# Performance work log

Measured on AMD Instinct MI355X. Metric: run time of the kernel, lower is better.

Reference implementation:

```python
import jax, jax.numpy as jnp
import numpy as np

B, N, D_IN = 128, 128, 1024
H1, D_OUT = 256, 32
K = 8  # num_clusters


def setup_inputs() -> dict:
    key = jax.random.key(0)
    ks = jax.random.split(key, 3)
    x = jax.random.normal(ks[0], (B, N, D_IN), dtype=jnp.float32)
    W1 = jax.random.normal(ks[1], (D_IN, H1), dtype=jnp.float32) * (1.0 / np.sqrt(D_IN))
    b1 = jnp.zeros((H1,), jnp.float32)
    W2 = jax.random.normal(ks[2], (H1, D_OUT), dtype=jnp.float32) * (1.0 / np.sqrt(H1))
    b2 = jnp.zeros((D_OUT,), jnp.float32)
    return {"x": x, "W1": W1, "b1": b1, "W2": W2, "b2": b2}


def _mlp(x, W1, b1, W2, b2):
    # nn.Sequential(GELU, Linear(1024,256), GELU, Linear(256,32)); torch GELU default = exact erf
    h = jax.nn.gelu(x, approximate=False)
    h = h @ W1 + b1
    h = jax.nn.gelu(h, approximate=False)
    return h @ W2 + b2  # [B, N, 32]


def _ward_labels(feats, k):
    """Greedy ward-linkage agglomerative clustering of feats [n, d] -> int labels [n].
    Ward merge cost d(A,B) = |A||B|/(|A|+|B|) * ||c_A - c_B||^2 (Lance-Williams equiv)."""
    n = feats.shape[0]
    eye = jnp.eye(n, dtype=bool)

    def body(t, state):
        cents, sizes, lab = state
        sq = jnp.sum(cents * cents, axis=-1)
        d2 = jnp.maximum(sq[:, None] + sq[None, :] - 2.0 * (cents @ cents.T), 0.0)
        w = (sizes[:, None] * sizes[None, :]) / (sizes[:, None] + sizes[None, :] + 1e-30)
        active = sizes > 0
        valid = (active[:, None] & active[None, :]) & (~eye)
        Dm = jnp.where(valid, w * d2, jnp.inf)
        idx = jnp.argmin(Dm)
        i, j = idx // n, idx % n
        i2 = jnp.minimum(i, j)
        j2 = jnp.maximum(i, j)
        si, sj = sizes[i2], sizes[j2]
        newc = (cents[i2] * si + cents[j2] * sj) / (si + sj)
        cents = cents.at[i2].set(newc)
        sizes = sizes.at[i2].set(si + sj).at[j2].set(0.0)
        lab = jnp.where(lab == j2, i2, lab)
        return cents, sizes, lab

    init = (feats, jnp.ones((n,), feats.dtype), jnp.arange(n))
    cents, sizes, lab = jax.lax.fori_loop(0, n - k, body, init)
    # relabel surviving representative indices to 0..k-1 (ordered by index)
    rank = jnp.cumsum((sizes > 0).astype(jnp.int32)) - 1
    return rank[lab]


def reference(x, W1, b1, W2, b2):
    feats = _mlp(x, W1, b1, W2, b2)          # [B, N, 32]
    labels = jax.vmap(lambda f: _ward_labels(f, K))(feats)  # [B, N] int32
    return labels
```

## Files before the change

kernel.cpp:

```cpp
#include <hip/hip_runtime.h>
#include <math.h>

#define BB 128
#define NN 128
#define DIN 1024
#define H1 256
#define DOUT 32
#define KCL 8
#define NPTS 128
#define MROWS (BB*NN)
#define CSTR 130
#define RSTR 132
#define DEADKEY 0xFFFFFFFF00000000ull

__device__ __forceinline__ float gelu_exact(float v) {
    return 0.5f * v * (1.0f + erff(v * 0.70710678118654752f));
}

__device__ __forceinline__ unsigned long long mkkey(float v, int r, int j) {
    return ((unsigned long long)__float_as_uint(v) << 32) | (unsigned)((r << 7) | j);
}

__device__ __forceinline__ float readlanef(float v, int lane) {
    return __int_as_float(__builtin_amdgcn_readlane(__float_as_int(v), lane));
}

template<int CTRL, int RMASK>
__device__ __forceinline__ unsigned dpp_umin_step(unsigned v) {
    unsigned t = (unsigned)__builtin_amdgcn_update_dpp((int)v, (int)v, CTRL, RMASK, 0xf, false);
    return t < v ? t : v;
}
__device__ __forceinline__ unsigned wave_umin_bcast(unsigned v) {
    v = dpp_umin_step<0x111, 0xf>(v);
    v = dpp_umin_step<0x112, 0xf>(v);
    v = dpp_umin_step<0x114, 0xf>(v);
    v = dpp_umin_step<0x118, 0xf>(v);
    v = dpp_umin_step<0x142, 0xa>(v);
    v = dpp_umin_step<0x143, 0xc>(v);
    return (unsigned)__builtin_amdgcn_readlane((int)v, 63);
}
__device__ __forceinline__ unsigned half_umin(unsigned v) {
    v = dpp_umin_step<0x111, 0xf>(v);
    v = dpp_umin_step<0x112, 0xf>(v);
    v = dpp_umin_step<0x114, 0xf>(v);
    v = dpp_umin_step<0x118, 0xf>(v);
    v = dpp_umin_step<0x142, 0xa>(v);
    return v;
}

__global__ __launch_bounds__(256) void gelu_kernel(const float* __restrict__ x,
                                                   float* __restrict__ gx, int n4) {
    int i = blockIdx.x * 256 + threadIdx.x;
    const int stride = gridDim.x * 256;
    for (; i < n4; i += stride) {
        float4 v = ((const float4*)x)[i];
        v.x = gelu_exact(v.x);
        v.y = gelu_exact(v.y);
        v.z = gelu_exact(v.z);
        v.w = gelu_exact(v.w);
        ((float4*)gx)[i] = v;
    }
}

template<bool FUSE>
__global__ __launch_bounds__(256) void mlp1_kernel(const float* __restrict__ xin,
                                                   const float* __restrict__ W1,
                                                   const float* __restrict__ b1,
                                                   float* __restrict__ h) {
    __shared__ float As[32][68];
    __shared__ float Bs[32][68];
    const int bm = blockIdx.x;
    const int bn = blockIdx.y;
    const int tid = threadIdx.x;
    const int tx = tid & 15, ty = tid >> 4;

    float acc[4][4] = {{0.f}};

    const int arow = tid >> 2;
    const int acol4 = (tid & 3) * 4;
    const int brow = tid >> 4;
    const int bcol4 = (tid & 15) * 4;

    const float* xrow = xin + (size_t)(bm * 64 + arow) * DIN;
    const float* wbase = W1 + bn * 64;

    for (int kt = 0; kt < DIN; kt += 32) {
        float4 a0 = *(const float4*)(xrow + kt + acol4);
        float4 a1 = *(const float4*)(xrow + kt + 16 + acol4);
        float4 w0 = *(const float4*)(wbase + (size_t)(kt + brow) * H1 + bcol4);
        float4 w1 = *(const float4*)(wbase + (size_t)(kt + 16 + brow) * H1 + bcol4);
        __syncthreads();
        if (FUSE) {
            As[acol4 + 0][arow] = gelu_exact(a0.x);
            As[acol4 + 1][arow] = gelu_exact(a0.y);
            As[acol4 + 2][arow] = gelu_exact(a0.z);
            As[acol4 + 3][arow] = gelu_exact(a0.w);
            As[16 + acol4 + 0][arow] = gelu_exact(a1.x);
            As[16 + acol4 + 1][arow] = gelu_exact(a1.y);
            As[16 + acol4 + 2][arow] = gelu_exact(a1.z);
            As[16 + acol4 + 3][arow] = gelu_exact(a1.w);
        } else {
            As[acol4 + 0][arow] = a0.x;
            As[acol4 + 1][arow] = a0.y;
            As[acol4 + 2][arow] = a0.z;
            As[acol4 + 3][arow] = a0.w;
            As[16 + acol4 + 0][arow] = a1.x;
            As[16 + acol4 + 1][arow] = a1.y;
            As[16 + acol4 + 2][arow] = a1.z;
            As[16 + acol4 + 3][arow] = a1.w;
        }
        *(float4*)&Bs[brow][bcol4] = w0;
        *(float4*)&Bs[16 + brow][bcol4] = w1;
        __syncthreads();
#pragma unroll
        for (int kk = 0; kk < 32; ++kk) {
            float4 a = *(const float4*)&As[kk][ty * 4];
            float4 b = *(const float4*)&Bs[kk][tx * 4];
            float ar[4] = {a.x, a.y, a.z, a.w};
            float br[4] = {b.x, b.y, b.z, b.w};
#pragma unroll
            for (int i = 0; i < 4; ++i)
#pragma unroll
                for (int j = 0; j < 4; ++j)
                    acc[i][j] = fmaf(ar[i], br[j], acc[i][j]);
        }
    }

    const int row = bm * 64 + ty * 4;
    const int col = bn * 64 + tx * 4;
    float4 bias = *(const float4*)(b1 + col);
#pragma unroll
    for (int i = 0; i < 4; ++i) {
        float4 o;
        o.x = acc[i][0] + bias.x;
        o.y = acc[i][1] + bias.y;
        o.z = acc[i][2] + bias.z;
        o.w = acc[i][3] + bias.w;
        *(float4*)(h + (size_t)(row + i) * H1 + col) = o;
    }
}

__global__ __launch_bounds__(256) void mlp2_kernel(const float* __restrict__ h,
                                                   const float* __restrict__ W2,
                                                   const float* __restrict__ b2,
                                                   float* __restrict__ feats) {
    __shared__ float hs[16][257];
    __shared__ float w2s[H1 * DOUT];
    const int blk = blockIdx.x;
    const int tid = threadIdx.x;

    for (int i = tid; i < (H1 * DOUT) / 4; i += 256) {
        ((float4*)w2s)[i] = ((const float4*)W2)[i];
    }
    const float* hb = h + (size_t)blk * 16 * H1;
    for (int i = tid; i < (16 * H1) / 4; i += 256) {
        float4 v = ((const float4*)hb)[i];
        int r = i >> 6;
        int c = (i & 63) * 4;
        hs[r][c + 0] = gelu_exact(v.x);
        hs[r][c + 1] = gelu_exact(v.y);
        hs[r][c + 2] = gelu_exact(v.z);
        hs[r][c + 3] = gelu_exact(v.w);
    }
    __syncthreads();

    const int col = tid & 31;
    const int r0 = (tid >> 5) * 2;
    float acc0 = 0.f, acc1 = 0.f;
    for (int k = 0; k < H1; ++k) {
        float w = w2s[k * DOUT + col];
        acc0 = fmaf(hs[r0 + 0][k], w, acc0);
        acc1 = fmaf(hs[r0 + 1][k], w, acc1);
    }
    float bias = b2[col];
    const int rowg = blk * 16 + r0;
    feats[(size_t)(rowg + 0) * DOUT + col] = acc0 + bias;
    feats[(size_t)(rowg + 1) * DOUT + col] = acc1 + bias;
}

__global__ __launch_bounds__(256) void ward_kernel(const float* __restrict__ feats,
                                                   int* __restrict__ out) {
    __shared__ __align__(16) float cost[NPTS * RSTR];
    __shared__ __align__(16) float G[NPTS * RSTR];
    __shared__ float centsT[32 * CSTR];
    __shared__ unsigned long long rowkey[NPTS];
    __shared__ float sqArr[NPTS];
    __shared__ float szsE[NPTS];
    __shared__ int rnk[NPTS];

    const int b = blockIdx.x;
    const int tid = threadIdx.x;
    const float* f = feats + (size_t)b * NPTS * DOUT;
    const float INF = __builtin_inff();

    for (int i = tid; i < NPTS * DOUT; i += 256) {
        int r = i >> 5, d = i & 31;
        centsT[d * CSTR + r] = f[i];
    }
    __syncthreads();
    if (tid < NPTS) {
        float s = 0.f;
#pragma unroll
        for (int d = 0; d < 32; ++d) {
            float v = centsT[d * CSTR + tid];
            s = fmaf(v, v, s);
        }
        sqArr[tid] = s;
    }
    __syncthreads();
    {
        int ti = tid >> 4, tj = tid & 15;
        int I0 = ti * 8, J0 = tj * 8;
        float acc[8][8];
#pragma unroll
        for (int u = 0; u < 8; ++u)
#pragma unroll
            for (int v = 0; v < 8; ++v) acc[u][v] = 0.f;
        for (int d = 0; d < 32; ++d) {
            float a[8], bb[8];
#pragma unroll
            for (int u = 0; u < 8; ++u) a[u] = centsT[d * CSTR + I0 + u];
#pragma unroll
            for (int v = 0; v < 8; ++v) bb[v] = centsT[d * CSTR + J0 + v];
#pragma unroll
            for (int u = 0; u < 8; ++u)
#pragma unroll
                for (int v = 0; v < 8; ++v)
                    acc[u][v] = fmaf(a[u], bb[v], acc[u][v]);
        }
#pragma unroll
        for (int u = 0; u < 8; ++u) {
#pragma unroll
            for (int v = 0; v < 8; ++v) {
                int i = I0 + u, j = J0 + v;
                G[i * RSTR + j] = acc[u][v];
                float d2 = sqArr[i] + sqArr[j] - 2.0f * acc[u][v];
                if (d2 < 0.f) d2 = 0.f;
                float w = (1.0f * 1.0f) / (1.0f + 1.0f + 1e-30f);
                cost[i * RSTR + j] = (i == j) ? INF : w * d2;
            }
        }
    }
    __syncthreads();
    if (tid < NPTS) {
        unsigned long long best = DEADKEY;
        for (int j = 0; j < NPTS; ++j) {
            float v = cost[tid * RSTR + j];
            unsigned long long k = mkkey(v, tid, j);
            if (k < best) best = k;
        }
        rowkey[tid] = best;
    }
    __syncthreads();

    if (tid >= 64) return;
    const int lane = tid;
    const int hh = lane & 31;
    const int r0 = lane * 2, r1 = lane * 2 + 1;

    unsigned long long k0 = rowkey[r0], k1 = rowkey[r1];
    float q0 = sqArr[r0], q1 = sqArr[r1];
    float s0 = 1.0f, s1 = 1.0f;
    int lab0 = r0, lab1 = r1;
    unsigned long long alive0 = ~0ull, alive1 = ~0ull;

    for (int it = 0; it < NPTS - KCL; ++it) {
        unsigned bv0 = (unsigned)(k0 >> 32), bv1 = (unsigned)(k1 >> 32);
        unsigned lmin = bv0 < bv1 ? bv0 : bv1;
        unsigned lflat = (bv0 <= bv1) ? (unsigned)(k0 & 0x3FFFu) : (unsigned)(k1 & 0x3FFFu);
        unsigned gmin = wave_umin_bcast(lmin);
        unsigned long long bmask = __ballot(lmin == gmin);
        int lsel = __ffsll(bmask) - 1;
        unsigned flat = (unsigned)__builtin_amdgcn_readlane((int)lflat, lsel);
        int ra = (int)(flat >> 7), ca = (int)(flat & 127u);
        const int i2 = ra < ca ? ra : ca;
        const int j2 = ra < ca ? ca : ra;

        float2 gi = *(const float2*)&G[i2 * RSTR + r0];
        float2 gj = *(const float2*)&G[j2 * RSTR + r0];

        float si = readlanef((i2 & 1) ? s1 : s0, i2 >> 1);
        float sj = readlanef((j2 & 1) ? s1 : s0, j2 >> 1);
        const float snew = si + sj;
        const float invs = 1.0f / snew;
        const float wa = si * invs, wb = sj * invs;

        int arg0 = (int)(k0 & 127u), arg1 = (int)(k1 & 127u);
        bool d0 = (s0 > 0.f) && r0 != i2 && r0 != j2 && (arg0 == i2 || arg0 == j2);
        bool d1 = (s1 > 0.f) && r1 != i2 && r1 != j2 && (arg1 == i2 || arg1 == j2);
        unsigned long long m0 = __ballot(d0), m1 = __ballot(d1);

        float Gii = readlanef((i2 & 1) ? gi.y : gi.x, i2 >> 1);
        float Gij = readlanef((i2 & 1) ? gj.y : gj.x, i2 >> 1);
        float Gjj = readlanef((j2 & 1) ? gj.y : gj.x, j2 >> 1);
        float dotA = wa * Gii + wb * Gij;
        float dotB = wa * Gij + wb * Gjj;
        float qn = wa * dotA + wb * dotB;

        float dot0 = wa * gi.x + wb * gj.x;
        float dot1 = wa * gi.y + wb * gj.y;

        if (lab0 == j2) lab0 = i2;
        if (lab1 == j2) lab1 = i2;
        if (r0 == i2) s0 = snew; else if (r0 == j2) { s0 = 0.f; k0 = DEADKEY; }
        if (r1 == i2) s1 = snew; else if (r1 == j2) { s1 = 0.f; k1 = DEADKEY; }
        if (j2 < 64) alive0 &= ~(1ull << j2); else alive1 &= ~(1ull << (j2 - 64));
        if (r0 == i2) { dot0 = qn; q0 = qn; }
        if (r1 == i2) { dot1 = qn; q1 = qn; }

        *(float2*)&G[i2 * RSTR + r0] = make_float2(dot0, dot1);
        G[r0 * RSTR + i2] = dot0;
        G[r1 * RSTR + i2] = dot1;

        bool w0 = (s0 > 0.f) && r0 != i2 && r0 != j2;
        bool w1 = (s1 > 0.f) && r1 != i2 && r1 != j2;
        if (w0) {
            float d2 = q0 + qn - 2.0f * dot0;
            if (d2 < 0.f) d2 = 0.f;
            float w = (s0 * snew) / (s0 + snew + 1e-30f);
            float v0 = w * d2;
            cost[r0 * RSTR + i2] = v0;
            cost[i2 * RSTR + r0] = v0;
            if (!d0) {
                unsigned long long nk = mkkey(v0, r0, i2);
                if (nk < k0) k0 = nk;
            }
        }
        if (w1) {
            float d2 = q1 + qn - 2.0f * dot1;
            if (d2 < 0.f) d2 = 0.f;
            float w = (s1 * snew) / (s1 + snew + 1e-30f);
            float v1 = w * d2;
            cost[r1 * RSTR + i2] = v1;
            cost[i2 * RSTR + r1] = v1;
            if (!d1) {
                unsigned long long nk = mkkey(v1, r1, i2);
                if (nk < k1) k1 = nk;
            }
        }

        bool pi = true;
        unsigned long long mm0 = m0, mm1 = m1;
        while (pi | (mm0 != 0ull) | (mm1 != 0ull)) {
            int rA, rB;
            bool hasB = false;
            if (pi) { rA = i2; pi = false; }
            else if (mm0) { int t = __ffsll(mm0) - 1; rA = 2 * t; mm0 &= mm0 - 1; }
            else { int t = __ffsll(mm1) - 1; rA = 2 * t + 1; mm1 &= mm1 - 1; }
            if (mm0) { int t = __ffsll(mm0) - 1; rB = 2 * t; mm0 &= mm0 - 1; hasB = true; }
            else if (mm1) { int t = __ffsll(mm1) - 1; rB = 2 * t + 1; mm1 &= mm1 - 1; hasB = true; }
            else rB = rA;

            int r = (lane < 32) ? rA : rB;
            float4 cv = *(const float4*)&cost[r * RSTR + 4 * hh];
            unsigned long long word = (hh < 16) ? alive0 : alive1;
            unsigned nib = (unsigned)(word >> ((4 * hh) & 63)) & 0xFu;
            unsigned e0 = (nib & 1u) ? __float_as_uint(cv.x) : 0xFFFFFFFFu;
            unsigned e1 = (nib & 2u) ? __float_as_uint(cv.y) : 0xFFFFFFFFu;
            unsigned e2 = (nib & 4u) ? __float_as_uint(cv.z) : 0xFFFFFFFFu;
            unsigned e3 = (nib & 8u) ? __float_as_uint(cv.w) : 0xFFFFFFFFu;
            unsigned m = e0; int c = 0;
            if (e1 < m) { m = e1; c = 1; }
            if (e2 < m) { m = e2; c = 2; }
            if (e3 < m) { m = e3; c = 3; }
            int lcol = 4 * hh + c;
            unsigned hm = half_umin(m);
            unsigned vA = (unsigned)__builtin_amdgcn_readlane((int)hm, 31);
            unsigned vB = (unsigned)__builtin_amdgcn_readlane((int)hm, 63);
            unsigned vref = (lane < 32) ? vA : vB;
            unsigned long long msk = __ballot(m == vref);
            int laneA = __ffsll(msk & 0xFFFFFFFFull) - 1;
            int laneB = 32 + __ffsll(msk >> 32) - 1;
            int colA = __builtin_amdgcn_readlane(lcol, laneA);
            int colB = __builtin_amdgcn_readlane(lcol, laneB);
            unsigned long long keyA = ((unsigned long long)vA << 32) | (unsigned)((rA << 7) | colA);
            unsigned long long keyB = ((unsigned long long)vB << 32) | (unsigned)((rB << 7) | colB);
            if (lane == (rA >> 1)) { if (rA & 1) k1 = keyA; else k0 = keyA; }
            if (hasB && lane == (rB >> 1)) { if (rB & 1) k1 = keyB; else k0 = keyB; }
        }
    }

    szsE[r0] = s0;
    szsE[r1] = s1;
    __asm__ volatile("s_waitcnt lgkmcnt(0)" ::: "memory");
    if (lane == 0) {
        int c = 0;
        for (int i = 0; i < NPTS; ++i) rnk[i] = (szsE[i] > 0.f) ? c++ : -1;
    }
    __asm__ volatile("s_waitcnt lgkmcnt(0)" ::: "memory");
    out[b * NPTS + r0] = rnk[lab0];
    out[b * NPTS + r1] = rnk[lab1];
}

extern "C" void kernel_launch(void* const* d_in, const int* in_sizes, int n_in,
                              void* d_out, int out_size, void* d_ws, size_t ws_size,
                              hipStream_t stream) {
    const float* x  = (const float*)d_in[0];
    const float* W1 = (const float*)d_in[1];
    const float* b1 = (const float*)d_in[2];
    const float* W2 = (const float*)d_in[3];
    const float* b2 = (const float*)d_in[4];

    float* h = (float*)d_ws;
    float* feats = h + (size_t)MROWS * H1;
    float* gx = feats + (size_t)MROWS * DOUT;
    int* out = (int*)d_out;

    const size_t need = ((size_t)MROWS * H1 + (size_t)MROWS * DOUT + (size_t)MROWS * DIN) * 4;
    const bool use_gx = ws_size >= need;

    if (use_gx) {
        gelu_kernel<<<2048, 256, 0, stream>>>(x, gx, MROWS * DIN / 4);
        mlp1_kernel<false><<<dim3(MROWS / 64, H1 / 64), 256, 0, stream>>>(gx, W1, b1, h);
    } else {
        mlp1_kernel<true><<<dim3(MROWS / 64, H1 / 64), 256, 0, stream>>>(x, W1, b1, h);
    }
    mlp2_kernel<<<MROWS / 16, 256, 0, stream>>>(h, W2, b2, feats);
    ward_kernel<<<BB, 256, 0, stream>>>(feats, out);
}
```

Measured before the change: 428.9 us.

## Enlarge GEMM tiles with register prefetch and track top-2 row minima in ward loop

The first MLP GEMM moves from 64x64 tiles with 4x4 per-thread outputs to 128x128 tiles with 8x8 outputs and a k-step of 16. It also prefetches the next tile's global loads into registers while the current tile is computed, so each loaded element is reused more and load latency overlaps the FMAs. Separately, the ward clustering loop now keeps a second-best key per row and recomputes the merged row's minimum with a wave-wide reduction, so fewer rows need a full rescan after each merge. In exchange the GEMM uses more registers, has lower occupancy and launches fewer blocks, and the top-2 bookkeeping adds per-iteration branching.

```diff
diff --git a/kernel.cpp b/kernel.cpp
--- a/kernel.cpp
+++ b/kernel.cpp
@@ -11,7 +11,8 @@
 #define MROWS (BB*NN)
 #define CSTR 130
 #define RSTR 132
-#define DEADKEY 0xFFFFFFFF00000000ull
+#define DEADKEY  0xFFFFFFFF00000000ull
+#define INVALIDK 0xFFFFFFFFFFFFFFFFull
 
 __device__ __forceinline__ float gelu_exact(float v) {
     return 0.5f * v * (1.0f + erff(v * 0.70710678118654752f));
@@ -46,6 +47,27 @@
     v = dpp_umin_step<0x118, 0xf>(v);
     v = dpp_umin_step<0x142, 0xa>(v);
     return v;
+}
+
+__device__ __forceinline__ void top2_update(unsigned long long &k, unsigned long long &kb,
+                                            bool &dirty, float v, int r, int i2, int j2) {
+    int ck = (int)(k & 127u);
+    bool pk = (ck == i2) || (ck == j2);
+    bool sval = (kb != INVALIDK);
+    int cs = (int)(kb & 127u);
+    bool ps = sval && ((cs == i2) || (cs == j2));
+    if (pk) {
+        if (sval && !ps) { k = kb; }
+        else { dirty = true; }
+        kb = INVALIDK;
+    } else if (ps) {
+        kb = INVALIDK;
+    }
+    if (!dirty) {
+        unsigned long long kn = mkkey(v, r, i2);
+        if (kn < k) { kb = k; k = kn; }
+        else if (kb != INVALIDK && kn < kb) kb = kn;
+    }
 }
 
 __global__ __launch_bounds__(256) void gelu_kernel(const float* __restrict__ x,
@@ -67,76 +89,97 @@
                                                    const float* __restrict__ W1,
                                                    const float* __restrict__ b1,
                                                    float* __restrict__ h) {
-    __shared__ float As[32][68];
-    __shared__ float Bs[32][68];
+    __shared__ float As[16][132];
+    __shared__ float Bs[16][132];
     const int bm = blockIdx.x;
     const int bn = blockIdx.y;
     const int tid = threadIdx.x;
-    const int tx = tid & 15, ty = tid >> 4;
-
-    float acc[4][4] = {{0.f}};
-
-    const int arow = tid >> 2;
-    const int acol4 = (tid & 3) * 4;
-    const int brow = tid >> 4;
-    const int bcol4 = (tid & 15) * 4;
-
-    const float* xrow = xin + (size_t)(bm * 64 + arow) * DIN;
-    const float* wbase = W1 + bn * 64;
-
-    for (int kt = 0; kt < DIN; kt += 32) {
-        float4 a0 = *(const float4*)(xrow + kt + acol4);
-        float4 a1 = *(const float4*)(xrow + kt + 16 + acol4);
-        float4 w0 = *(const float4*)(wbase + (size_t)(kt + brow) * H1 + bcol4);
-        float4 w1 = *(const float4*)(wbase + (size_t)(kt + 16 + brow) * H1 + bcol4);
+    const int tx = tid & 15;
+    const int ty = tid >> 4;
+
+    float acc[8][8];
+#pragma unroll
+    for (int i = 0; i < 8; ++i)
+#pragma unroll
+        for (int j = 0; j < 8; ++j) acc[i][j] = 0.f;
+
+    const int arow = tid >> 1;
+    const int ak8  = (tid & 1) * 8;
+    const int bk   = tid >> 4;
+    const int bcol = (tid & 15) * 8;
+
+    const float* xrow = xin + (size_t)(bm * 128 + arow) * DIN;
+    const float* wbase = W1 + bn * 128;
+
+    float4 a0 = *(const float4*)(xrow + ak8);
+    float4 a1 = *(const float4*)(xrow + ak8 + 4);
+    float4 w0 = *(const float4*)(wbase + (size_t)bk * H1 + bcol);
+    float4 w1 = *(const float4*)(wbase + (size_t)bk * H1 + bcol + 4);
+
+    for (int kt = 0; kt < DIN; kt += 16) {
         __syncthreads();
         if (FUSE) {
-            As[acol4 + 0][arow] = gelu_exact(a0.x);
-            As[acol4 + 1][arow] = gelu_exact(a0.y);
-            As[acol4 + 2][arow] = gelu_exact(a0.z);
-            As[acol4 + 3][arow] = gelu_exact(a0.w);
-            As[16 + acol4 + 0][arow] = gelu_exact(a1.x);
-            As[16 + acol4 + 1][arow] = gelu_exact(a1.y);
-            As[16 + acol4 + 2][arow] = gelu_exact(a1.z);
-            As[16 + acol4 + 3][arow] = gelu_exact(a1.w);
+            As[ak8 + 0][arow] = gelu_exact(a0.x);
+            As[ak8 + 1][arow] = gelu_exact(a0.y);
+            As[ak8 + 2][arow] = gelu_exact(a0.z);
+            As[ak8 + 3][arow] = gelu_exact(a0.w);
+            As[ak8 + 4][arow] = gelu_exact(a1.x);
+            As[ak8 + 5][arow] = gelu_exact(a1.y);
+            As[ak8 + 6][arow] = gelu_exact(a1.z);
+            As[ak8 + 7][arow] = gelu_exact(a1.w);
         } else {
-            As[acol4 + 0][arow] = a0.x;
-            As[acol4 + 1][arow] = a0.y;
-            As[acol4 + 2][arow] = a0.z;
-            As[acol4 + 3][arow] = a0.w;
-            As[16 + acol4 + 0][arow] = a1.x;
-            As[16 + acol4 + 1][arow] = a1.y;
-            As[16 + acol4 + 2][arow] = a1.z;
-            As[16 + acol4 + 3][arow] = a1.w;
-        }
-        *(float4*)&Bs[brow][bcol4] = w0;
-        *(float4*)&Bs[16 + brow][bcol4] = w1;
+            As[ak8 + 0][arow] = a0.x;
+            As[ak8 + 1][arow] = a0.y;
+            As[ak8 + 2][arow] = a0.z;
+            As[ak8 + 3][arow] = a0.w;
+            As[ak8 + 4][arow] = a1.x;
+            As[ak8 + 5][arow] = a1.y;
+            As[ak8 + 6][arow] = a1.z;
+            As[ak8 + 7][arow] = a1.w;
+        }
+        *(float4*)&Bs[bk][bcol] = w0;
+        *(float4*)&Bs[bk][bcol + 4] = w1;
         __syncthreads();
-#pragma unroll
-        for (int kk = 0; kk < 32; ++kk) {
-            float4 a = *(const float4*)&As[kk][ty * 4];
-            float4 b = *(const float4*)&Bs[kk][tx * 4];
-            float ar[4] = {a.x, a.y, a.z, a.w};
-            float br[4] = {b.x, b.y, b.z, b.w};
-#pragma unroll
-            for (int i = 0; i < 4; ++i)
-#pragma unroll
-                for (int j = 0; j < 4; ++j)
+        if (kt + 16 < DIN) {
+            a0 = *(const float4*)(xrow + kt + 16 + ak8);
+            a1 = *(const float4*)(xrow + kt + 16 + ak8 + 4);
+            w0 = *(const float4*)(wbase + (size_t)(kt + 16 + bk) * H1 + bcol);
+            w1 = *(const float4*)(wbase + (size_t)(kt + 16 + bk) * H1 + bcol + 4);
+        }
+#pragma unroll
+        for (int kk = 0; kk < 16; ++kk) {
+            float4 aL = *(const float4*)&As[kk][ty * 4];
+            float4 aH = *(const float4*)&As[kk][64 + ty * 4];
+            float4 bL = *(const float4*)&Bs[kk][tx * 4];
+            float4 bH = *(const float4*)&Bs[kk][64 + tx * 4];
+            float ar[8] = {aL.x, aL.y, aL.z, aL.w, aH.x, aH.y, aH.z, aH.w};
+            float br[8] = {bL.x, bL.y, bL.z, bL.w, bH.x, bH.y, bH.z, bH.w};
+#pragma unroll
+            for (int i = 0; i < 8; ++i)
+#pragma unroll
+                for (int j = 0; j < 8; ++j)
                     acc[i][j] = fmaf(ar[i], br[j], acc[i][j]);
         }
     }
 
-    const int row = bm * 64 + ty * 4;
-    const int col = bn * 64 + tx * 4;
-    float4 bias = *(const float4*)(b1 + col);
-#pragma unroll
-    for (int i = 0; i < 4; ++i) {
-        float4 o;
-        o.x = acc[i][0] + bias.x;
-        o.y = acc[i][1] + bias.y;
-        o.z = acc[i][2] + bias.z;
-        o.w = acc[i][3] + bias.w;
-        *(float4*)(h + (size_t)(row + i) * H1 + col) = o;
+    const int row0 = bm * 128 + ty * 4;
+    const int col0 = bn * 128 + tx * 4;
+    float4 biasL = *(const float4*)(b1 + col0);
+    float4 biasH = *(const float4*)(b1 + col0 + 64);
+#pragma unroll
+    for (int i = 0; i < 8; ++i) {
+        int rr = (i < 4) ? i : (64 + i - 4);
+        float4 oL, oH;
+        oL.x = acc[i][0] + biasL.x;
+        oL.y = acc[i][1] + biasL.y;
+        oL.z = acc[i][2] + biasL.z;
+        oL.w = acc[i][3] + biasL.w;
+        oH.x = acc[i][4] + biasH.x;
+        oH.y = acc[i][5] + biasH.y;
+        oH.z = acc[i][6] + biasH.z;
+        oH.w = acc[i][7] + biasH.w;
+        *(float4*)(h + (size_t)(row0 + rr) * H1 + col0) = oL;
+        *(float4*)(h + (size_t)(row0 + rr) * H1 + col0 + 64) = oH;
     }
 }
 
@@ -184,6 +227,7 @@
     __shared__ __align__(16) float G[NPTS * RSTR];
     __shared__ float centsT[32 * CSTR];
     __shared__ unsigned long long rowkey[NPTS];
+    __shared__ unsigned long long rowsec[NPTS];
     __shared__ float sqArr[NPTS];
     __shared__ float szsE[NPTS];
     __shared__ int rnk[NPTS];
@@ -243,13 +287,22 @@
     }
     __syncthreads();
     if (tid < NPTS) {
-        unsigned long long best = DEADKEY;
-        for (int j = 0; j < NPTS; ++j) {
-            float v = cost[tid * RSTR + j];
-            unsigned long long k = mkkey(v, tid, j);
-            if (k < best) best = k;
+        unsigned long long best = INVALIDK, sec = INVALIDK;
+        const float* cr = &cost[tid * RSTR];
+        for (int j4 = 0; j4 < NPTS / 4; ++j4) {
+            float4 v = *(const float4*)(cr + 4 * j4);
+            unsigned long long kx;
+            kx = mkkey(v.x, tid, 4 * j4 + 0);
+            if (kx < best) { sec = best; best = kx; } else if (kx < sec) sec = kx;
+            kx = mkkey(v.y, tid, 4 * j4 + 1);
+            if (kx < best) { sec = best; best = kx; } else if (kx < sec) sec = kx;
+            kx = mkkey(v.z, tid, 4 * j4 + 2);
+            if (kx < best) { sec = best; best = kx; } else if (kx < sec) sec = kx;
+            kx = mkkey(v.w, tid, 4 * j4 + 3);
+            if (kx < best) { sec = best; best = kx; } else if (kx < sec) sec = kx;
         }
         rowkey[tid] = best;
+        rowsec[tid] = sec;
     }
     __syncthreads();
 
@@ -259,6 +312,7 @@
     const int r0 = lane * 2, r1 = lane * 2 + 1;
 
     unsigned long long k0 = rowkey[r0], k1 = rowkey[r1];
+    unsigned long long k0b = rowsec[r0], k1b = rowsec[r1];
     float q0 = sqArr[r0], q1 = sqArr[r1];
     float s0 = 1.0f, s1 = 1.0f;
     int lab0 = r0, lab1 = r1;
@@ -285,11 +339,6 @@
         const float invs = 1.0f / snew;
         const float wa = si * invs, wb = sj * invs;
 
-        int arg0 = (int)(k0 & 127u), arg1 = (int)(k1 & 127u);
-        bool d0 = (s0 > 0.f) && r0 != i2 && r0 != j2 && (arg0 == i2 || arg0 == j2);
-        bool d1 = (s1 > 0.f) && r1 != i2 && r1 != j2 && (arg1 == i2 || arg1 == j2);
-        unsigned long long m0 = __ballot(d0), m1 = __ballot(d1);
-
         float Gii = readlanef((i2 & 1) ? gi.y : gi.x, i2 >> 1);
         float Gij = readlanef((i2 & 1) ? gj.y : gj.x, i2 >> 1);
         float Gjj = readlanef((j2 & 1) ? gj.y : gj.x, j2 >> 1);
@@ -302,8 +351,8 @@
 
         if (lab0 == j2) lab0 = i2;
         if (lab1 == j2) lab1 = i2;
-        if (r0 == i2) s0 = snew; else if (r0 == j2) { s0 = 0.f; k0 = DEADKEY; }
-        if (r1 == i2) s1 = snew; else if (r1 == j2) { s1 = 0.f; k1 = DEADKEY; }
+        if (r0 == i2) s0 = snew; else if (r0 == j2) { s0 = 0.f; k0 = DEADKEY; k0b = INVALIDK; }
+        if (r1 == i2) s1 = snew; else if (r1 == j2) { s1 = 0.f; k1 = DEADKEY; k1b = INVALIDK; }
         if (j2 < 64) alive0 &= ~(1ull << j2); else alive1 &= ~(1ull << (j2 - 64));
         if (r0 == i2) { dot0 = qn; q0 = qn; }
         if (r1 == i2) { dot1 = qn; q1 = qn; }
@@ -314,38 +363,51 @@
 
         bool w0 = (s0 > 0.f) && r0 != i2 && r0 != j2;
         bool w1 = (s1 > 0.f) && r1 != i2 && r1 != j2;
+        float v0 = 0.f, v1 = 0.f;
+        unsigned uv0 = 0xFFFFFFFFu, uv1 = 0xFFFFFFFFu;
         if (w0) {
             float d2 = q0 + qn - 2.0f * dot0;
             if (d2 < 0.f) d2 = 0.f;
             float w = (s0 * snew) / (s0 + snew + 1e-30f);
-            float v0 = w * d2;
+            v0 = w * d2;
             cost[r0 * RSTR + i2] = v0;
             cost[i2 * RSTR + r0] = v0;
-            if (!d0) {
-                unsigned long long nk = mkkey(v0, r0, i2);
-                if (nk < k0) k0 = nk;
-            }
+            uv0 = __float_as_uint(v0);
         }
         if (w1) {
             float d2 = q1 + qn - 2.0f * dot1;
             if (d2 < 0.f) d2 = 0.f;
             float w = (s1 * snew) / (s1 + snew + 1e-30f);
-            float v1 = w * d2;
+            v1 = w * d2;
             cost[r1 * RSTR + i2] = v1;
             cost[i2 * RSTR + r1] = v1;
-            if (!d1) {
-                unsigned long long nk = mkkey(v1, r1, i2);
-                if (nk < k1) k1 = nk;
+            uv1 = __float_as_uint(v1);
+        }
+
+        {
+            unsigned vm = uv0 < uv1 ? uv0 : uv1;
+            int cm = (uv0 <= uv1) ? r0 : r1;
+            unsigned gm2 = wave_umin_bcast(vm);
+            unsigned long long bm2 = __ballot(vm == gm2);
+            int ls2 = __ffsll(bm2) - 1;
+            int ccol = __builtin_amdgcn_readlane(cm, ls2);
+            unsigned long long ki2 =
+                ((unsigned long long)gm2 << 32) | (unsigned)((i2 << 7) | ccol);
+            if (lane == (i2 >> 1)) {
+                if (i2 & 1) { k1 = ki2; k1b = INVALIDK; }
+                else        { k0 = ki2; k0b = INVALIDK; }
             }
         }
 
-        bool pi = true;
-        unsigned long long mm0 = m0, mm1 = m1;
-        while (pi | (mm0 != 0ull) | (mm1 != 0ull)) {
+        bool dirty0 = false, dirty1 = false;
+        if (w0) top2_update(k0, k0b, dirty0, v0, r0, i2, j2);
+        if (w1) top2_update(k1, k1b, dirty1, v1, r1, i2, j2);
+        unsigned long long mm0 = __ballot(dirty0), mm1 = __ballot(dirty1);
+
+        while (mm0 | mm1) {
             int rA, rB;
             bool hasB = false;
-            if (pi) { rA = i2; pi = false; }
-            else if (mm0) { int t = __ffsll(mm0) - 1; rA = 2 * t; mm0 &= mm0 - 1; }
+            if (mm0) { int t = __ffsll(mm0) - 1; rA = 2 * t; mm0 &= mm0 - 1; }
             else { int t = __ffsll(mm1) - 1; rA = 2 * t + 1; mm1 &= mm1 - 1; }
             if (mm0) { int t = __ffsll(mm0) - 1; rB = 2 * t; mm0 &= mm0 - 1; hasB = true; }
             else if (mm1) { int t = __ffsll(mm1) - 1; rB = 2 * t + 1; mm1 &= mm1 - 1; hasB = true; }
@@ -411,9 +473,9 @@
 
     if (use_gx) {
         gelu_kernel<<<2048, 256, 0, stream>>>(x, gx, MROWS * DIN / 4);
-        mlp1_kernel<false><<<dim3(MROWS / 64, H1 / 64), 256, 0, stream>>>(gx, W1, b1, h);
+        mlp1_kernel<false><<<dim3(MROWS / 128, H1 / 128), 256, 0, stream>>>(gx, W1, b1, h);
     } else {
-        mlp1_kernel<true><<<dim3(MROWS / 64, H1 / 64), 256, 0, stream>>>(x, W1, b1, h);
+        mlp1_kernel<true><<<dim3(MROWS / 128, H1 / 128), 256, 0, stream>>>(x, W1, b1, h);
     }
     mlp2_kernel<<<MROWS / 16, 256, 0, stream>>>(h, W2, b2, feats);
     ward_kernel<<<BB, 256, 0, stream>>>(feats, out);
```

Measured after the change: 502.3 us. 1.17x slower.
